# Kernel tuning notes

Measured on AMD Instinct MI355X. Metric: run time of the kernel, lower is better.

The kernel has to match this reference:

```python
import jax, jax.numpy as jnp
import numpy as np

B = 131072
UNITS = 256
INPUT_DIM = 256


def setup_inputs() -> dict:
    key = jax.random.key(0)
    ks = jax.random.split(key, 8)
    x = jax.random.normal(ks[0], (B, INPUT_DIM), dtype=jnp.float32)
    h_prev = jax.random.normal(ks[1], (B, UNITS), dtype=jnp.float32)
    c_prev = jax.random.normal(ks[2], (B, UNITS), dtype=jnp.float32)
    # glorot-like scale for W: fan_in = INPUT_DIM + UNITS, fan_out = 4*UNITS
    scale = jnp.sqrt(2.0 / (INPUT_DIM + UNITS + 4 * UNITS)).astype(jnp.float32)
    W = jax.random.normal(ks[3], (INPUT_DIM + UNITS, 4 * UNITS), dtype=jnp.float32) * scale
    # bias: zeros except forget gate initialized to 1.0
    b = jnp.concatenate([
        jnp.zeros(UNITS, jnp.float32),
        jnp.ones(UNITS, jnp.float32),
        jnp.zeros(UNITS, jnp.float32),
        jnp.zeros(UNITS, jnp.float32),
    ])
    peephole_i = jax.random.normal(ks[4], (UNITS,), dtype=jnp.float32) * 0.05
    peephole_f = jax.random.normal(ks[5], (UNITS,), dtype=jnp.float32) * 0.05
    peephole_o = jax.random.normal(ks[6], (UNITS,), dtype=jnp.float32) * 0.05
    return {
        "x": x, "h_prev": h_prev, "c_prev": c_prev,
        "W": W, "b": b,
        "peephole_i": peephole_i, "peephole_f": peephole_f, "peephole_o": peephole_o,
    }


def reference(x, h_prev, c_prev, W, b, peephole_i, peephole_f, peephole_o):
    combined = jnp.concatenate([x, h_prev], axis=-1)          # [B, INPUT_DIM+UNITS]
    z = combined @ W + b                                      # [B, 4*UNITS]
    i, f, c_hat, o = jnp.split(z, 4, axis=1)                  # each [B, UNITS]
    i = jax.nn.sigmoid(i + peephole_i * c_prev)
    f = jax.nn.sigmoid(f + peephole_f * c_prev)
    o = jax.nn.sigmoid(o + peephole_o * c_prev)
    c_hat = jnp.tanh(c_hat)
    c = f * c_prev + i * c_hat
    h = o * jnp.tanh(c)
    return (h, h, c)  # matches (output, [h, c]) of the Keras cell
```

## Files before the change

kernel.cpp:

```cpp
#include <hip/hip_runtime.h>
#include <cstdint>

#define NROWS   131072
#define NUNITS  256
#define KTOT    512
#define BM      128
#define THREADS 512

typedef float f32x4  __attribute__((ext_vector_type(4)));
typedef short bf16x8 __attribute__((ext_vector_type(8)));

__device__ __forceinline__ short f2bf(float x) {
    unsigned u = __float_as_uint(x);
    u += 0x7FFFu + ((u >> 16) & 1u);
    return (short)(u >> 16);
}

__global__ void convert_W_kernel(const float* __restrict__ W, short* __restrict__ Wws) {
    int i = blockIdx.x * 256 + threadIdx.x;
    int k = i >> 10;
    int c = i & 1023;
    Wws[((size_t)(k >> 5) << 15) + ((size_t)c << 5) + (k & 31)] = f2bf(W[i]);
}

__global__ void __launch_bounds__(THREADS, 4)
lstm_main_kernel(const float* __restrict__ x, const float* __restrict__ h_prev,
                 const float* __restrict__ c_prev, const float* __restrict__ bias,
                 const float* __restrict__ pi, const float* __restrict__ pf,
                 const float* __restrict__ po, const short* __restrict__ Wws,
                 float* __restrict__ out) {
    __shared__ float Alds[3][4096];
    __shared__ short Blds[2][8192];

    const int bid = blockIdx.x;
    const int swz = (bid & 7) * 512 + (bid >> 3);
    const int ut  = swz & 3;
    const int rt  = swz >> 2;
    const int row0 = rt * BM;

    const int t    = threadIdx.x;
    const int lane = t & 63;
    const int w    = t >> 6;
    const int lr   = lane & 15;
    const int hi   = lane >> 4;
    const int rh   = w >> 2;
    const int q    = w & 3;

    const float* aX[2]; const float* aH[2];
    #pragma unroll
    for (int rep = 0; rep < 2; ++rep) {
        const int G = rep * 512 + t;
        const int r = G >> 3, s = G & 7, g = s ^ (r & 7);
        aX[rep] = x      + (size_t)(row0 + r) * 256 + g * 4;
        aH[rep] = h_prev + (size_t)(row0 + r) * 256 + g * 4;
    }
    const short* srcB[2];
    #pragma unroll
    for (int rep = 0; rep < 2; ++rep) {
        const int G = rep * 512 + t;
        const int cp = G >> 2, bg = G & 3;
        const int gate = cp >> 6, u64 = cp & 63;
        srcB[rep] = Wws + (size_t)(gate * 256 + ut * 64 + u64) * 32
                        + ((bg ^ ((cp >> 1) & 3)) * 8);
    }

    const int s0    = (2 * hi) ^ (lr & 7);
    const int bsw   = (hi ^ ((lr >> 1) & 3)) * 8;
    const int boff  = (q * 16 + lr) * 32 + bsw;

    f32x4 acc[4][4];
    #pragma unroll
    for (int m = 0; m < 4; ++m)
        #pragma unroll
        for (int g = 0; g < 4; ++g)
            acc[m][g] = (f32x4){0.f, 0.f, 0.f, 0.f};

    auto dmaA = [&](int ks, int buf) {
        const int off = (ks & 7) * 32;
        const float* p0 = (ks < 8 ? aX[0] : aH[0]) + off;
        const float* p1 = (ks < 8 ? aX[1] : aH[1]) + off;
        float* dst = &Alds[buf][0];
        __builtin_amdgcn_global_load_lds(
            (const __attribute__((address_space(1))) uint32_t*)(const void*)p0,
            (__attribute__((address_space(3))) uint32_t*)(void*)(dst + t * 4), 16, 0, 0);
        __builtin_amdgcn_global_load_lds(
            (const __attribute__((address_space(1))) uint32_t*)(const void*)p1,
            (__attribute__((address_space(3))) uint32_t*)(void*)(dst + 2048 + t * 4), 16, 0, 0);
    };
    auto dmaB = [&](int ks, int buf) {
        short* dst = &Blds[buf][0];
        __builtin_amdgcn_global_load_lds(
            (const __attribute__((address_space(1))) uint32_t*)(const void*)(srcB[0] + (size_t)ks * 32768),
            (__attribute__((address_space(3))) uint32_t*)(void*)(dst + t * 8), 16, 0, 0);
        __builtin_amdgcn_global_load_lds(
            (const __attribute__((address_space(1))) uint32_t*)(const void*)(srcB[1] + (size_t)ks * 32768),
            (__attribute__((address_space(3))) uint32_t*)(void*)(dst + 4096 + t * 8), 16, 0, 0);
    };

    auto compute = [&](int abuf, int bbuf) {
        const float* A = &Alds[abuf][0];
        const short* B = &Blds[bbuf][0];
        bf16x8 af[4], bfr[4];
        #pragma unroll
        for (int m = 0; m < 4; ++m) {
            const int r = rh * 64 + m * 16 + lr;
            f32x4 lo = *(const f32x4*)&A[r * 32 + s0 * 4];
            f32x4 hi4 = *(const f32x4*)&A[r * 32 + (s0 ^ 1) * 4];
            unsigned u0, u1, u2, u3;
            asm("v_cvt_pk_bf16_f32 %0, %1, %2" : "=v"(u0) : "v"(lo[0]),  "v"(lo[1]));
            asm("v_cvt_pk_bf16_f32 %0, %1, %2" : "=v"(u1) : "v"(lo[2]),  "v"(lo[3]));
            asm("v_cvt_pk_bf16_f32 %0, %1, %2" : "=v"(u2) : "v"(hi4[0]), "v"(hi4[1]));
            asm("v_cvt_pk_bf16_f32 %0, %1, %2" : "=v"(u3) : "v"(hi4[2]), "v"(hi4[3]));
            unsigned uu[4] = {u0, u1, u2, u3};
            af[m] = *(bf16x8*)uu;
        }
        #pragma unroll
        for (int g = 0; g < 4; ++g)
            bfr[g] = *(const bf16x8*)&B[boff + g * 2048];
        __builtin_amdgcn_s_setprio(1);
        #pragma unroll
        for (int g = 0; g < 4; ++g)
            #pragma unroll
            for (int m = 0; m < 4; ++m)
                acc[m][g] = __builtin_amdgcn_mfma_f32_16x16x32_bf16(af[m], bfr[g], acc[m][g], 0, 0, 0);
        __builtin_amdgcn_s_setprio(0);
    };

    dmaA(0, 0);
    dmaB(0, 0);
    dmaA(1, 1);

    int ab = 0;
    #pragma unroll 1
    for (int p = 0; p < 16; ++p) {
        if (p < 15) { asm volatile("s_waitcnt vmcnt(2)" ::: "memory"); }
        else        { asm volatile("s_waitcnt vmcnt(0)" ::: "memory"); }
        __builtin_amdgcn_s_barrier();
        if (p < 15) dmaB(p + 1, (p + 1) & 1);
        if (p < 14) { int nb = ab + 2; if (nb >= 3) nb -= 3; dmaA(p + 2, nb); }
        compute(ab, p & 1);
        if (++ab == 3) ab = 0;
    }

    const size_t HS = (size_t)NROWS * NUNITS;
    const int u = ut * 64 + q * 16 + lr;
    const float bi = bias[u],       bfg = bias[256 + u];
    const float bc = bias[512 + u], bo  = bias[768 + u];
    const float ppi = pi[u], ppf = pf[u], ppo = po[u];
    #pragma unroll
    for (int m = 0; m < 4; ++m) {
        #pragma unroll
        for (int r = 0; r < 4; ++r) {
            const int row = row0 + rh * 64 + m * 16 + hi * 4 + r;
            const size_t o = (size_t)row * NUNITS + u;
            const float cp = c_prev[o];
            float zi = acc[m][0][r] + bi  + ppi * cp;
            float zf = acc[m][1][r] + bfg + ppf * cp;
            float zc = acc[m][2][r] + bc;
            float zo = acc[m][3][r] + bo  + ppo * cp;
            float ig = 1.f / (1.f + __expf(-zi));
            float fg = 1.f / (1.f + __expf(-zf));
            float og = 1.f / (1.f + __expf(-zo));
            zc = fminf(fmaxf(zc, -30.f), 30.f);
            float e2 = __expf(2.f * zc);
            float chat = (e2 - 1.f) / (e2 + 1.f);
            float c  = fg * cp + ig * chat;
            float ccl = fminf(fmaxf(c, -30.f), 30.f);
            float e3 = __expf(2.f * ccl);
            float th = (e3 - 1.f) / (e3 + 1.f);
            float h  = og * th;
            out[o]          = h;
            out[HS + o]     = h;
            out[2 * HS + o] = c;
        }
    }
}

extern "C" void kernel_launch(void* const* d_in, const int* in_sizes, int n_in,
                              void* d_out, int out_size, void* d_ws, size_t ws_size,
                              hipStream_t stream) {
    const float* x  = (const float*)d_in[0];
    const float* h  = (const float*)d_in[1];
    const float* c  = (const float*)d_in[2];
    const float* W  = (const float*)d_in[3];
    const float* b  = (const float*)d_in[4];
    const float* pi = (const float*)d_in[5];
    const float* pf = (const float*)d_in[6];
    const float* po = (const float*)d_in[7];
    float* out = (float*)d_out;

    short* Wws = (short*)d_ws;

    hipLaunchKernelGGL(convert_W_kernel, dim3(2048), dim3(256), 0, stream, W, Wws);
    hipLaunchKernelGGL(lstm_main_kernel, dim3(NROWS / BM * 4), dim3(THREADS), 0, stream,
                       x, h, c, b, pi, pf, po, Wws, out);
}
```

Before: 322.2 us.

## Convert A tiles to bf16 in registers before LDS store; triple-buffer W

The A operand (x/h_prev) is now loaded from global memory into registers, converted to bf16 once per element, and written to LDS as bf16. Previously fp32 was DMA'd directly to LDS and reconverted inside each wave's compute. This halves LDS footprint and LDS read traffic for A and removes the redundant conversions done by the four waves that share a row block. W now uses a three-stage LDS ring and A a two-stage ring, with one barrier per iteration placed after the A write. The trade-off is that A global-load latency is exposed through registers instead of async DMA, and register pressure rises.

```diff
diff --git a/kernel.cpp b/kernel.cpp
--- a/kernel.cpp
+++ b/kernel.cpp
@@ -29,8 +29,8 @@
                  const float* __restrict__ pi, const float* __restrict__ pf,
                  const float* __restrict__ po, const short* __restrict__ Wws,
                  float* __restrict__ out) {
-    __shared__ float Alds[3][4096];
-    __shared__ short Blds[2][8192];
+    __shared__ short Ab[2][4096];
+    __shared__ short Bb[3][8192];
 
     const int bid = blockIdx.x;
     const int swz = (bid & 7) * 512 + (bid >> 3);
@@ -46,27 +46,19 @@
     const int rh   = w >> 2;
     const int q    = w & 3;
 
-    const float* aX[2]; const float* aH[2];
-    #pragma unroll
-    for (int rep = 0; rep < 2; ++rep) {
-        const int G = rep * 512 + t;
-        const int r = G >> 3, s = G & 7, g = s ^ (r & 7);
-        aX[rep] = x      + (size_t)(row0 + r) * 256 + g * 4;
-        aH[rep] = h_prev + (size_t)(row0 + r) * 256 + g * 4;
-    }
-    const short* srcB[2];
-    #pragma unroll
-    for (int rep = 0; rep < 2; ++rep) {
-        const int G = rep * 512 + t;
-        const int cp = G >> 2, bg = G & 3;
-        const int gate = cp >> 6, u64 = cp & 63;
-        srcB[rep] = Wws + (size_t)(gate * 256 + ut * 64 + u64) * 32
-                        + ((bg ^ ((cp >> 1) & 3)) * 8);
-    }
+    const int arow = t >> 2, ag = t & 3;
+    const int avoff = ((row0 + arow) * 256 + ag * 8) * 4;
+    const int awr   = arow * 32 + ((ag ^ ((arow >> 1) & 3)) * 8);
 
-    const int s0    = (2 * hi) ^ (lr & 7);
-    const int bsw   = (hi ^ ((lr >> 1) & 3)) * 8;
-    const int boff  = (q * 16 + lr) * 32 + bsw;
+    const int u0  = (t >> 2) & 63;
+    const int bg0 = t >> 8;
+    const int bsw = ((t & 3) ^ ((t >> 3) & 3)) * 8;
+    const int bvoff0 = (((bg0    ) * 256 + ut * 64 + u0) * 32 + bsw) * 2;
+    const int bvoff1 = (((bg0 + 2) * 256 + ut * 64 + u0) * 32 + bsw) * 2;
+
+    const int sw   = (hi ^ ((lr >> 1) & 3)) * 8;
+    const int aoff = (rh * 64 + lr) * 32 + sw;
+    const int boff = (q * 16 + lr) * 32 + sw;
 
     f32x4 acc[4][4];
     #pragma unroll
@@ -75,45 +67,38 @@
         for (int g = 0; g < 4; ++g)
             acc[m][g] = (f32x4){0.f, 0.f, 0.f, 0.f};
 
-    auto dmaA = [&](int ks, int buf) {
-        const int off = (ks & 7) * 32;
-        const float* p0 = (ks < 8 ? aX[0] : aH[0]) + off;
-        const float* p1 = (ks < 8 ? aX[1] : aH[1]) + off;
-        float* dst = &Alds[buf][0];
+    f32x4 sreg[2];
+    auto glbA = [&](int p) {
+        const char* base = (const char*)(p < 8 ? x : h_prev) + ((p & 7) << 7);
+        sreg[0] = *(const f32x4*)(base + avoff);
+        sreg[1] = *(const f32x4*)(base + avoff + 16);
+    };
+    auto writeA = [&](int buf) {
+        unsigned u0_, u1_, u2_, u3_;
+        asm("v_cvt_pk_bf16_f32 %0, %1, %2" : "=v"(u0_) : "v"(sreg[0][0]), "v"(sreg[0][1]));
+        asm("v_cvt_pk_bf16_f32 %0, %1, %2" : "=v"(u1_) : "v"(sreg[0][2]), "v"(sreg[0][3]));
+        asm("v_cvt_pk_bf16_f32 %0, %1, %2" : "=v"(u2_) : "v"(sreg[1][0]), "v"(sreg[1][1]));
+        asm("v_cvt_pk_bf16_f32 %0, %1, %2" : "=v"(u3_) : "v"(sreg[1][2]), "v"(sreg[1][3]));
+        int4 v = make_int4((int)u0_, (int)u1_, (int)u2_, (int)u3_);
+        *(int4*)&Ab[buf][awr] = v;
+    };
+    auto dmaB = [&](int p, int buf) {
+        const char* wb = (const char*)Wws + ((size_t)p << 16);
+        short* dst = &Bb[buf][0];
         __builtin_amdgcn_global_load_lds(
-            (const __attribute__((address_space(1))) uint32_t*)(const void*)p0,
-            (__attribute__((address_space(3))) uint32_t*)(void*)(dst + t * 4), 16, 0, 0);
-        __builtin_amdgcn_global_load_lds(
-            (const __attribute__((address_space(1))) uint32_t*)(const void*)p1,
-            (__attribute__((address_space(3))) uint32_t*)(void*)(dst + 2048 + t * 4), 16, 0, 0);
-    };
-    auto dmaB = [&](int ks, int buf) {
-        short* dst = &Blds[buf][0];
-        __builtin_amdgcn_global_load_lds(
-            (const __attribute__((address_space(1))) uint32_t*)(const void*)(srcB[0] + (size_t)ks * 32768),
+            (const __attribute__((address_space(1))) uint32_t*)(const void*)(wb + bvoff0),
             (__attribute__((address_space(3))) uint32_t*)(void*)(dst + t * 8), 16, 0, 0);
         __builtin_amdgcn_global_load_lds(
-            (const __attribute__((address_space(1))) uint32_t*)(const void*)(srcB[1] + (size_t)ks * 32768),
+            (const __attribute__((address_space(1))) uint32_t*)(const void*)(wb + bvoff1),
             (__attribute__((address_space(3))) uint32_t*)(void*)(dst + 4096 + t * 8), 16, 0, 0);
     };
-
-    auto compute = [&](int abuf, int bbuf) {
-        const float* A = &Alds[abuf][0];
-        const short* B = &Blds[bbuf][0];
+    auto compute = [&](int bufA, int bufB) {
+        const short* A = &Ab[bufA][0];
+        const short* B = &Bb[bufB][0];
         bf16x8 af[4], bfr[4];
         #pragma unroll
-        for (int m = 0; m < 4; ++m) {
-            const int r = rh * 64 + m * 16 + lr;
-            f32x4 lo = *(const f32x4*)&A[r * 32 + s0 * 4];
-            f32x4 hi4 = *(const f32x4*)&A[r * 32 + (s0 ^ 1) * 4];
-            unsigned u0, u1, u2, u3;
-            asm("v_cvt_pk_bf16_f32 %0, %1, %2" : "=v"(u0) : "v"(lo[0]),  "v"(lo[1]));
-            asm("v_cvt_pk_bf16_f32 %0, %1, %2" : "=v"(u1) : "v"(lo[2]),  "v"(lo[3]));
-            asm("v_cvt_pk_bf16_f32 %0, %1, %2" : "=v"(u2) : "v"(hi4[0]), "v"(hi4[1]));
-            asm("v_cvt_pk_bf16_f32 %0, %1, %2" : "=v"(u3) : "v"(hi4[2]), "v"(hi4[3]));
-            unsigned uu[4] = {u0, u1, u2, u3};
-            af[m] = *(bf16x8*)uu;
-        }
+        for (int m = 0; m < 4; ++m)
+            af[m] = *(const bf16x8*)&A[aoff + m * 512];
         #pragma unroll
         for (int g = 0; g < 4; ++g)
             bfr[g] = *(const bf16x8*)&B[boff + g * 2048];
@@ -126,20 +111,25 @@
         __builtin_amdgcn_s_setprio(0);
     };
 
-    dmaA(0, 0);
+    glbA(0);
     dmaB(0, 0);
-    dmaA(1, 1);
+    dmaB(1, 1);
+    writeA(0);
+    asm volatile("s_waitcnt vmcnt(2) lgkmcnt(0)" ::: "memory");
+    __builtin_amdgcn_s_barrier();
 
-    int ab = 0;
-    #pragma unroll 1
+    #pragma unroll 2
     for (int p = 0; p < 16; ++p) {
-        if (p < 15) { asm volatile("s_waitcnt vmcnt(2)" ::: "memory"); }
-        else        { asm volatile("s_waitcnt vmcnt(0)" ::: "memory"); }
-        __builtin_amdgcn_s_barrier();
-        if (p < 15) dmaB(p + 1, (p + 1) & 1);
-        if (p < 14) { int nb = ab + 2; if (nb >= 3) nb -= 3; dmaA(p + 2, nb); }
-        compute(ab, p & 1);
-        if (++ab == 3) ab = 0;
+        const int ca = p & 1, na = ca ^ 1;
+        if (p < 15) glbA(p + 1);
+        if (p < 14) dmaB(p + 2, (p + 2) % 3);
+        compute(ca, p % 3);
+        if (p < 15) {
+            writeA(na);
+            if (p < 14) { asm volatile("s_waitcnt vmcnt(2) lgkmcnt(0)" ::: "memory"); }
+            else        { asm volatile("s_waitcnt vmcnt(0) lgkmcnt(0)" ::: "memory"); }
+            __builtin_amdgcn_s_barrier();
+        }
     }
 
     const size_t HS = (size_t)NROWS * NUNITS;
```

Measured after the change: 307.7 us. 4.5% less time.
